# Kernel optimization log

Measured on AMD Instinct MI355X. Metric: run time of the kernel, lower is better.

## Reference

```python
import jax, jax.numpy as jnp
import numpy as np


def setup_inputs() -> dict:
    key = jax.random.key(0)
    kx, kw = jax.random.split(key)
    B, IN, OUT = 8192, 4096, 4096
    x = jax.random.normal(kx, (B, IN), dtype=jnp.float32)
    # matches torch init: (rand*2-1)*0.001 -> uniform in [-0.001, 0.001]
    weight = jax.random.uniform(kw, (OUT, IN), dtype=jnp.float32, minval=-1.0, maxval=1.0) * 0.001
    return {"x": x, "weight": weight}


def reference(x, weight):
    # scaling factor = mean(|W|), detached
    scale = jax.lax.stop_gradient(jnp.mean(jnp.abs(weight)))
    binary_no_grad = scale * jnp.sign(weight)
    clipped = jnp.clip(weight, -1.0, 1.0)
    # straight-through estimator: fwd value = scale*sign(W), bwd grad = d(clip)/dW
    binary_weights = jax.lax.stop_gradient(binary_no_grad - clipped) + clipped
    # F.linear: y = x @ W^T  -> [B, OUT]
    return jnp.einsum('bi,oi->bo', x, binary_weights)
```

## Files before the change

### kernel.cpp

```cpp
#include <hip/hip_runtime.h>
#include <hip/hip_bf16.h>
#include <stdint.h>

typedef __attribute__((ext_vector_type(4))) int i32x4;

#define GLOAD(g, l) __builtin_amdgcn_global_load_lds(                      \
    (const __attribute__((address_space(1))) void*)(g),                    \
    (__attribute__((address_space(3))) void*)(l), 16, 0, 0)

#define MFMAI8 __builtin_amdgcn_mfma_i32_16x16x64_i8
#define BARRIER __builtin_amdgcn_s_barrier
#define LGKM0 asm volatile("s_waitcnt lgkmcnt(0)" ::: "memory")

__global__ __launch_bounds__(256) void wsign_kernel(
    const float* __restrict__ W, char* __restrict__ S,
    float* __restrict__ partials) {
  const int tid = threadIdx.x;
  const int idx = blockIdx.x * 256 + tid;
  const float4* wp = reinterpret_cast<const float4*>(W) + (size_t)idx * 4;
  float s = 0.f;
  int out[4];
#pragma unroll
  for (int i = 0; i < 4; ++i) {
    float4 w = wp[i];
    int b0 = (w.x > 0.f) - (w.x < 0.f);
    int b1 = (w.y > 0.f) - (w.y < 0.f);
    int b2 = (w.z > 0.f) - (w.z < 0.f);
    int b3 = (w.w > 0.f) - (w.w < 0.f);
    out[i] = (b0 & 255) | ((b1 & 255) << 8) | ((b2 & 255) << 16) |
             ((b3 & 255) << 24);
    s += fabsf(w.x) + fabsf(w.y) + fabsf(w.z) + fabsf(w.w);
  }
  reinterpret_cast<int4*>(S)[idx] =
      make_int4(out[0], out[1], out[2], out[3]);
#pragma unroll
  for (int off = 32; off > 0; off >>= 1) s += __shfl_down(s, off, 64);
  __shared__ float sm[4];
  if ((tid & 63) == 0) sm[tid >> 6] = s;
  __syncthreads();
  if (tid == 0) partials[blockIdx.x] = sm[0] + sm[1] + sm[2] + sm[3];
}

__global__ __launch_bounds__(256) void xquant_kernel(
    const float* __restrict__ X, char* __restrict__ XQ,
    float* __restrict__ qrow) {
  const int row = blockIdx.x;
  const int tid = threadIdx.x;
  const float4* xr = reinterpret_cast<const float4*>(X + (size_t)row * 4096);
  float4 v[4];
  float am = 0.f;
#pragma unroll
  for (int i = 0; i < 4; ++i) {
    v[i] = xr[tid * 4 + i];
    am = fmaxf(am, fmaxf(fmaxf(fabsf(v[i].x), fabsf(v[i].y)),
                         fmaxf(fabsf(v[i].z), fabsf(v[i].w))));
  }
#pragma unroll
  for (int off = 1; off < 64; off <<= 1)
    am = fmaxf(am, __shfl_xor(am, off, 64));
  __shared__ float wm[4];
  if ((tid & 63) == 0) wm[tid >> 6] = am;
  __syncthreads();
  float amax = fmaxf(fmaxf(wm[0], wm[1]), fmaxf(wm[2], wm[3]));
  amax = fmaxf(amax, 1e-20f);
  const float rq = 127.f / amax;
  int out[4];
#pragma unroll
  for (int i = 0; i < 4; ++i) {
    int b0 = __float2int_rn(v[i].x * rq);
    int b1 = __float2int_rn(v[i].y * rq);
    int b2 = __float2int_rn(v[i].z * rq);
    int b3 = __float2int_rn(v[i].w * rq);
    out[i] = (b0 & 255) | ((b1 & 255) << 8) | ((b2 & 255) << 16) |
             ((b3 & 255) << 24);
  }
  reinterpret_cast<int4*>(XQ + (size_t)row * 4096)[tid] =
      make_int4(out[0], out[1], out[2], out[3]);
  if (tid == 0) qrow[row] = amax * (1.f / 127.f);
}

__global__ __launch_bounds__(256) void finalize_kernel(
    const float* __restrict__ partials, float* __restrict__ scale) {
  const int tid = threadIdx.x;
  float s = 0.f;
  for (int i = tid; i < 4096; i += 256) s += partials[i];
#pragma unroll
  for (int off = 32; off > 0; off >>= 1) s += __shfl_down(s, off, 64);
  __shared__ float sm[4];
  if ((tid & 63) == 0) sm[tid >> 6] = s;
  __syncthreads();
  if (tid == 0) scale[0] = (sm[0] + sm[1] + sm[2] + sm[3]) * (1.0f / 16777216.0f);
}

__global__ __launch_bounds__(512, 2) void gemm_i8_kernel(
    const char* __restrict__ A,
    const char* __restrict__ B,
    const float* __restrict__ scale_p, const float* __restrict__ qrow,
    float* __restrict__ C) {
  constexpr int M = 8192, N = 4096, K = 4096;
  constexpr int NT = K / 128;
  constexpr int NI = NT / 2;
  __shared__ __align__(16) char lds[131072];

  const int tid = threadIdx.x;
  const int wid = tid >> 6;
  const int lane = tid & 63;
  const int wr = wid >> 2;
  const int wc = wid & 3;
  const int bh = wc >> 1;
  const int bsub = (wc & 1) * 8192;
  const int fr = lane & 15;
  const int fq = lane >> 4;
  const int sk0 = ((fq) ^ (fr & 7)) * 16;
  const int sk1 = ((4 + fq) ^ (fr & 7)) * 16;

  const int bid = blockIdx.x;
  const int swz = (bid & 7) * 64 + (bid >> 3);
  const int tm = swz >> 4, tn = swz & 15;

  const int srow = tid >> 3;
  const int sg = (tid & 7) ^ (srow & 7);
  const char* aSrc0 = A + (size_t)(tm * 256 + srow) * K + sg * 16;
  const char* aSrc1 = aSrc0 + (size_t)128 * K;
  const char* bSrc0 = B + (size_t)(tn * 256 + srow) * K + sg * 16;
  const char* bSrc1 = bSrc0 + (size_t)128 * K;

#define STAGE(srcBase, slotIdx, koff)                              \
  do {                                                             \
    const char* _s = (srcBase) + (koff);                           \
    char* _d = lds + (slotIdx) * 16384 + wid * 1024;               \
    GLOAD(_s, _d);                                                 \
    GLOAD(_s + (size_t)64 * K, _d + 8192);                         \
  } while (0)

  const char* aSp0 = lds + (0 + wr) * 16384 + fr * 128;
  const char* aSp1 = lds + (2 + wr) * 16384 + fr * 128;
  const char* bSp0 = lds + (4 + bh) * 16384 + bsub + fr * 128;
  const char* bSp1 = lds + (6 + bh) * 16384 + bsub + fr * 128;

  i32x4 acc[8][4];
#pragma unroll
  for (int m = 0; m < 8; ++m)
#pragma unroll
    for (int n = 0; n < 4; ++n) acc[m][n] = (i32x4){0, 0, 0, 0};

#define RD_B(bS)                                                       \
  _Pragma("unroll") for (int n = 0; n < 4; ++n) {                      \
    bq[n][0] = *(const i32x4*)((bS) + n * 2048 + sk0);                 \
    bq[n][1] = *(const i32x4*)((bS) + n * 2048 + sk1);                 \
  }
#define RD_A(aS, q)                                                    \
  _Pragma("unroll") for (int m2 = 0; m2 < 2; ++m2) {                   \
    av[m2][0] = *(const i32x4*)((aS) + (2 * (q) + m2) * 2048 + sk0);   \
    av[m2][1] = *(const i32x4*)((aS) + (2 * (q) + m2) * 2048 + sk1);   \
  }
#define QMFMA(q)                                                       \
  do {                                                                 \
    __builtin_amdgcn_s_setprio(1);                                     \
    _Pragma("unroll") for (int m2 = 0; m2 < 2; ++m2)                   \
        _Pragma("unroll") for (int n = 0; n < 4; ++n) {                \
      acc[2 * (q) + m2][n] =                                           \
          MFMAI8(av[m2][0], bq[n][0], acc[2 * (q) + m2][n], 0, 0, 0);  \
      acc[2 * (q) + m2][n] =                                           \
          MFMAI8(av[m2][1], bq[n][1], acc[2 * (q) + m2][n], 0, 0, 0);  \
    }                                                                  \
    __builtin_amdgcn_s_setprio(0);                                     \
  } while (0)

  STAGE(bSrc0, 4, 0);
  STAGE(bSrc1, 5, 0);
  STAGE(aSrc0, 0, 0);
  STAGE(aSrc1, 1, 0);
  STAGE(bSrc0, 6, 128);
  STAGE(bSrc1, 7, 128);
  asm volatile("s_waitcnt vmcnt(4)" ::: "memory");
  BARRIER();

  for (int i = 0; i < NI; ++i) {
    const int t0 = 2 * i;
    const int k1 = (t0 + 1) * 128, k2 = (t0 + 2) * 128, k3 = (t0 + 3) * 128;
    i32x4 bq[4][2], av[2][2];

    RD_B(bSp0);
    RD_A(aSp0, 0);
    STAGE(aSrc0, 2, k1);
    LGKM0; BARRIER(); QMFMA(0);

    RD_A(aSp0, 1);
    STAGE(aSrc1, 3, k1);
    LGKM0; BARRIER(); QMFMA(1);

    RD_A(aSp0, 2);
    if (t0 + 2 < NT) STAGE(bSrc0, 4, k2);
    LGKM0; BARRIER(); QMFMA(2);

    RD_A(aSp0, 3);
    if (t0 + 2 < NT) {
      STAGE(bSrc1, 5, k2);
      asm volatile("s_waitcnt vmcnt(4)" ::: "memory");
    } else {
      asm volatile("s_waitcnt vmcnt(0)" ::: "memory");
    }
    LGKM0; BARRIER(); QMFMA(3);

    RD_B(bSp1);
    RD_A(aSp1, 0);
    if (t0 + 2 < NT) STAGE(aSrc0, 0, k2);
    LGKM0; BARRIER(); QMFMA(0);

    RD_A(aSp1, 1);
    if (t0 + 2 < NT) STAGE(aSrc1, 1, k2);
    LGKM0; BARRIER(); QMFMA(1);

    RD_A(aSp1, 2);
    if (t0 + 3 < NT) STAGE(bSrc0, 6, k3);
    LGKM0; BARRIER(); QMFMA(2);

    RD_A(aSp1, 3);
    if (t0 + 3 < NT) {
      STAGE(bSrc1, 7, k3);
      asm volatile("s_waitcnt vmcnt(4)" ::: "memory");
    }
    LGKM0; BARRIER(); QMFMA(3);
  }

  const float sc = *scale_p;
  const int crow0 = tm * 256 + wr * 128 + fq * 4;
  const int ccol0 = tn * 256 + wc * 64 + fr;
#pragma unroll
  for (int m = 0; m < 8; ++m) {
    const int row = crow0 + m * 16;
    float q[4];
#pragma unroll
    for (int j = 0; j < 4; ++j) q[j] = sc * qrow[row + j];
#pragma unroll
    for (int n = 0; n < 4; ++n) {
      i32x4 v = acc[m][n];
      float* cp = C + (size_t)row * N + ccol0 + n * 16;
#pragma unroll
      for (int j = 0; j < 4; ++j) cp[(size_t)j * N] = (float)v[j] * q[j];
    }
  }
#undef STAGE
#undef RD_A
#undef RD_B
#undef QMFMA
}

extern "C" void kernel_launch(void* const* d_in, const int* in_sizes, int n_in,
                              void* d_out, int out_size, void* d_ws,
                              size_t ws_size, hipStream_t stream) {
  const float* x = (const float*)d_in[0];
  const float* w = (const float*)d_in[1];
  float* out = (float*)d_out;

  char* ws = (char*)d_ws;
  char* xq = ws;
  char* sq = ws + 33554432;
  float* qrow = (float*)(ws + 50331648);
  float* partials = (float*)(ws + 50331648 + 32768);
  float* scale = (float*)(ws + 50331648 + 32768 + 16384);

  wsign_kernel<<<4096, 256, 0, stream>>>(w, sq, partials);
  xquant_kernel<<<8192, 256, 0, stream>>>(x, xq, qrow);
  finalize_kernel<<<1, 256, 0, stream>>>(partials, scale);
  gemm_i8_kernel<<<512, 512, 0, stream>>>(xq, sq, scale, qrow, out);
}
```

Baseline: 176.1 us.

## Simplify int8 GEMM main loop to per-tile double buffering with two barriers

Replaces the hand-interleaved two-tile loop in the int8 GEMM kernel with a single-tile loop (unrolled by 2) that alternates between two LDS buffers by tile parity. Each iteration prefetches the next A tile and the tile-after-next B tile, then runs all MFMAs for the current tile. The aim is to drop the eight per-quarter barriers and explicit lgkmcnt waits, leaving two barriers per tile and letting the compiler schedule LDS reads around the MFMAs. In exchange, the fine-grained interleaving of global loads with MFMA quarters is lost, so latency hiding now depends on compiler scheduling.

```diff
diff --git a/kernel.cpp b/kernel.cpp
--- a/kernel.cpp
+++ b/kernel.cpp
@@ -10,7 +10,6 @@
 
 #define MFMAI8 __builtin_amdgcn_mfma_i32_16x16x64_i8
 #define BARRIER __builtin_amdgcn_s_barrier
-#define LGKM0 asm volatile("s_waitcnt lgkmcnt(0)" ::: "memory")
 
 __global__ __launch_bounds__(256) void wsign_kernel(
     const float* __restrict__ W, char* __restrict__ S,
@@ -99,7 +98,6 @@
     float* __restrict__ C) {
   constexpr int M = 8192, N = 4096, K = 4096;
   constexpr int NT = K / 128;
-  constexpr int NI = NT / 2;
   __shared__ __align__(16) char lds[131072];
 
   const int tid = threadIdx.x;
@@ -133,10 +131,8 @@
     GLOAD(_s + (size_t)64 * K, _d + 8192);                         \
   } while (0)
 
-  const char* aSp0 = lds + (0 + wr) * 16384 + fr * 128;
-  const char* aSp1 = lds + (2 + wr) * 16384 + fr * 128;
-  const char* bSp0 = lds + (4 + bh) * 16384 + bsub + fr * 128;
-  const char* bSp1 = lds + (6 + bh) * 16384 + bsub + fr * 128;
+  const char* aSp0 = lds + wr * 16384 + fr * 128;
+  const char* bSp0 = lds + 65536 + bh * 16384 + bsub + fr * 128;
 
   i32x4 acc[8][4];
 #pragma unroll
@@ -176,52 +172,39 @@
   asm volatile("s_waitcnt vmcnt(4)" ::: "memory");
   BARRIER();
 
-  for (int i = 0; i < NI; ++i) {
-    const int t0 = 2 * i;
-    const int k1 = (t0 + 1) * 128, k2 = (t0 + 2) * 128, k3 = (t0 + 3) * 128;
+#pragma unroll 2
+  for (int t = 0; t < NT; ++t) {
+    const int par = t & 1;
+    const char* aS = aSp0 + par * 32768;
+    const char* bS = bSp0 + par * 32768;
+    const int k1 = (t + 1) * 128, k2 = (t + 2) * 128;
+
+    if (t + 1 < NT) {
+      STAGE(aSrc0, (par ^ 1) * 2, k1);
+      STAGE(aSrc1, (par ^ 1) * 2 + 1, k1);
+    }
+
     i32x4 bq[4][2], av[2][2];
-
-    RD_B(bSp0);
-    RD_A(aSp0, 0);
-    STAGE(aSrc0, 2, k1);
-    LGKM0; BARRIER(); QMFMA(0);
-
-    RD_A(aSp0, 1);
-    STAGE(aSrc1, 3, k1);
-    LGKM0; BARRIER(); QMFMA(1);
-
-    RD_A(aSp0, 2);
-    if (t0 + 2 < NT) STAGE(bSrc0, 4, k2);
-    LGKM0; BARRIER(); QMFMA(2);
-
-    RD_A(aSp0, 3);
-    if (t0 + 2 < NT) {
-      STAGE(bSrc1, 5, k2);
+    RD_B(bS);
+    RD_A(aS, 0);
+    QMFMA(0);
+    RD_A(aS, 1);
+    QMFMA(1);
+    RD_A(aS, 2);
+    QMFMA(2);
+    RD_A(aS, 3);
+    QMFMA(3);
+
+    BARRIER();
+
+    if (t + 2 < NT) {
+      STAGE(bSrc0, 4 + par * 2, k2);
+      STAGE(bSrc1, 4 + par * 2 + 1, k2);
       asm volatile("s_waitcnt vmcnt(4)" ::: "memory");
     } else {
       asm volatile("s_waitcnt vmcnt(0)" ::: "memory");
     }
-    LGKM0; BARRIER(); QMFMA(3);
-
-    RD_B(bSp1);
-    RD_A(aSp1, 0);
-    if (t0 + 2 < NT) STAGE(aSrc0, 0, k2);
-    LGKM0; BARRIER(); QMFMA(0);
-
-    RD_A(aSp1, 1);
-    if (t0 + 2 < NT) STAGE(aSrc1, 1, k2);
-    LGKM0; BARRIER(); QMFMA(1);
-
-    RD_A(aSp1, 2);
-    if (t0 + 3 < NT) STAGE(bSrc0, 6, k3);
-    LGKM0; BARRIER(); QMFMA(2);
-
-    RD_A(aSp1, 3);
-    if (t0 + 3 < NT) {
-      STAGE(bSrc1, 7, k3);
-      asm volatile("s_waitcnt vmcnt(4)" ::: "memory");
-    }
-    LGKM0; BARRIER(); QMFMA(3);
+    if (t < NT - 1) BARRIER();
   }
 
   const float sc = *scale_p;
```

Measured after the change: 182.9 us. 1.04x slower.
